# Optimization experiments

Measured on AMD Instinct MI355X. Metric: run time of the kernel, lower is better.

The kernel has to match this reference:

```python
import jax, jax.numpy as jnp
import numpy as np

N = 100000   # nodes
E = 3200000  # edges
G = 256      # graphs in batch
C_IN, H, OUT = 5, 64, 2
EPS = 1e-5


def setup_inputs() -> dict:
    key = jax.random.key(0)
    ks = jax.random.split(key, 16)
    d = {
        "x": jax.random.normal(ks[0], (N, C_IN), jnp.float32),
        "edge_index": jax.random.randint(ks[1], (2, E), 0, N, jnp.int64),
        "batch": jnp.sort(jax.random.randint(ks[2], (N,), 0, G, jnp.int64)),
        "W1": jax.random.normal(ks[3], (C_IN, H), jnp.float32),
        "b1": jax.random.normal(ks[4], (H,), jnp.float32),
        "g1": jax.random.uniform(ks[5], (H,), jnp.float32),
        "be1": jax.random.normal(ks[6], (H,), jnp.float32),
        "rm1": jnp.zeros((H,), jnp.float32),
        "rv1": jnp.ones((H,), jnp.float32),
        "W2": jax.random.normal(ks[7], (H, H), jnp.float32),
        "b2": jax.random.normal(ks[8], (H,), jnp.float32),
        "g2": jax.random.uniform(ks[9], (H,), jnp.float32),
        "be2": jax.random.normal(ks[10], (H,), jnp.float32),
        "rm2": jnp.zeros((H,), jnp.float32),
        "rv2": jnp.ones((H,), jnp.float32),
        "W3": jax.random.normal(ks[11], (H, H), jnp.float32),
        "b3": jax.random.normal(ks[12], (H,), jnp.float32),
        "g3": jax.random.uniform(ks[13], (H,), jnp.float32),
        "be3": jax.random.normal(ks[14], (H,), jnp.float32),
        "rm3": jnp.zeros((H,), jnp.float32),
        "rv3": jnp.ones((H,), jnp.float32),
        "Wf1": jax.random.normal(ks[15], (H, 32), jnp.float32),
        "bf1": jax.random.normal(jax.random.fold_in(key, 1), (32,), jnp.float32),
        "Wf2": jax.random.normal(jax.random.fold_in(key, 2), (32, OUT), jnp.float32),
        "bf2": jax.random.normal(jax.random.fold_in(key, 3), (OUT,), jnp.float32),
    }
    return d


def reference(x, edge_index, batch, W1, b1, g1, be1, rm1, rv1,
              W2, b2, g2, be2, rm2, rv2, W3, b3, g3, be3, rm3, rv3,
              Wf1, bf1, Wf2, bf2):
    src, dst = edge_index[0], edge_index[1]
    # GCN symmetric normalization with self-loops: deg includes the self edge
    deg = jax.ops.segment_sum(jnp.ones((E,), x.dtype), dst, num_segments=N) + 1.0
    dinv = jax.lax.rsqrt(deg)            # [N]
    enorm = dinv[src] * dinv[dst]        # per-edge norm  [E]
    snorm = dinv * dinv                  # self-loop norm [N]

    def gcn(h, W, b):
        h = h @ W                                                  # [N,H]
        agg = jax.ops.segment_sum(h[src] * enorm[:, None], dst, num_segments=N)
        return agg + h * snorm[:, None] + b

    def bn(h, g, be, rm, rv):  # eval-mode BatchNorm1d
        return (h - rm) * jax.lax.rsqrt(rv + EPS) * g + be

    h = jax.nn.relu(bn(gcn(x, W1, b1), g1, be1, rm1, rv1))
    h = jax.nn.relu(bn(gcn(h, W2, b2), g2, be2, rm2, rv2))
    h = jax.nn.relu(bn(gcn(h, W3, b3), g3, be3, rm3, rv3))

    counts = jax.ops.segment_sum(jnp.ones((N,), h.dtype), batch, num_segments=G)
    pooled = jax.ops.segment_sum(h, batch, num_segments=G) / jnp.maximum(counts, 1.0)[:, None]

    h = jax.nn.relu(pooled @ Wf1 + bf1)  # dropout is identity in eval
    return jax.nn.sigmoid(h @ Wf2 + bf2)
```

## Files before the change

### kernel.cpp

```cpp
#include <hip/hip_runtime.h>
#include <hip/hip_bf16.h>

#define HF 64
#define EPS 1e-5f

#define BSH 9
#define BKN (1 << BSH)
#define NBUCK_MAX 256
#define PB_T 256
#define PB_EPT 32
#define PB_TILE (PB_T * PB_EPT)

#define LGRID 2048

typedef __hip_bfloat16 bf16;

__device__ __forceinline__ unsigned char f32_to_fp8(float v) {
    int p = __builtin_amdgcn_cvt_pk_fp8_f32(v, v, 0, false);
    return (unsigned char)(p & 0xff);
}

__device__ __forceinline__ float rdlane(float v, int k) {
    return __int_as_float(__builtin_amdgcn_readlane(__float_as_int(v), k));
}

__device__ __forceinline__ unsigned bf16_rne_hi(float x) {
    unsigned u = __float_as_uint(x);
    return (u + 0x7fffu + ((u >> 16) & 1u)) & 0xffff0000u;
}

__global__ __launch_bounds__(PB_T) void k_bhist(const int* __restrict__ dst,
                                                int* __restrict__ bcnt, int E, int B) {
    __shared__ int bh[NBUCK_MAX];
    int t = threadIdx.x;
    for (int b = t; b < B; b += PB_T) bh[b] = 0;
    __syncthreads();
    int tile0 = blockIdx.x * PB_TILE;
#pragma unroll
    for (int k = 0; k < PB_EPT; ++k) {
        int e = tile0 + k * PB_T + t;
        if (e < E) atomicAdd(&bh[dst[e] >> BSH], 1);
    }
    __syncthreads();
    for (int b = t; b < B; b += PB_T) {
        int c = bh[b];
        if (c) atomicAdd(&bcnt[b], c);
    }
}

__global__ void k_bscan(const int* __restrict__ bcnt, int* __restrict__ bbase2,
                        int* __restrict__ bcur, int* __restrict__ base, int B, int N, int E) {
    if (threadIdx.x == 0 && blockIdx.x == 0) {
        int acc = 0;
        for (int i = 0; i < B; ++i) { bbase2[i] = acc; bcur[i] = acc; acc += bcnt[i]; }
        bbase2[B] = acc;
        base[N] = E;
    }
}

__global__ __launch_bounds__(PB_T) void k_passB(
    const int* __restrict__ src, const int* __restrict__ dst,
    int* __restrict__ bcur, int* __restrict__ stage, int E, int B) {
    __shared__ int scnt[NBUCK_MAX];
    __shared__ int sgoff[NBUCK_MAX];
    int t = threadIdx.x;
    int tile0 = blockIdx.x * PB_TILE;

    for (int b = t; b < B; b += PB_T) scnt[b] = 0;
    __syncthreads();

    int rec[PB_EPT];
    int bkt[PB_EPT];
#pragma unroll
    for (int k = 0; k < PB_EPT; ++k) {
        int e = tile0 + k * PB_T + t;
        bkt[k] = -1;
        if (e < E) {
            int d = dst[e];
            int s = src[e];
            int b = d >> BSH;
            bkt[k] = b;
            rec[k] = s | ((d & (BKN - 1)) << 17);
            atomicAdd(&scnt[b], 1);
        }
    }
    __syncthreads();

    for (int b = t; b < B; b += PB_T) {
        int c = scnt[b];
        sgoff[b] = c ? atomicAdd(&bcur[b], c) : 0;
        scnt[b] = 0;
    }
    __syncthreads();

#pragma unroll
    for (int k = 0; k < PB_EPT; ++k) {
        if (bkt[k] >= 0) {
            int loc = atomicAdd(&scnt[bkt[k]], 1);
            stage[sgoff[bkt[k]] + loc] = rec[k];
        }
    }
}

__global__ __launch_bounds__(512) void k_passC(const int* __restrict__ stage,
                                               const int* __restrict__ bb2,
                                               int* __restrict__ base,
                                               float* __restrict__ dinv,
                                               int* __restrict__ csr, int N) {
    __shared__ int lcnt[BKN];
    __shared__ int lscan[BKN];
    __shared__ int lcur[BKN];
    int beta = blockIdx.x;
    int n0 = beta * BKN;
    int n1 = n0 + BKN; if (n1 > N) n1 = N;
    int nn = n1 - n0;
    int t = threadIdx.x;
    lcnt[t] = 0;
    __syncthreads();
    int rbeg = bb2[beta], rend = bb2[beta + 1];
    for (int i = rbeg + t; i < rend; i += 512)
        atomicAdd(&lcnt[stage[i] >> 17], 1);
    __syncthreads();
    int v = lcnt[t];
    lscan[t] = v;
    __syncthreads();
    for (int off = 1; off < 512; off <<= 1) {
        int val = lscan[t];
        int add = (t >= off) ? lscan[t - off] : 0;
        __syncthreads();
        lscan[t] = val + add;
        __syncthreads();
    }
    int b = rbeg + lscan[t] - v;
    if (t < nn) {
        base[n0 + t] = b;
        dinv[n0 + t] = rsqrtf((float)v + 1.0f);
    }
    lcur[t] = b;
    __syncthreads();
    for (int i = rbeg + t; i < rend; i += 512) {
        int r = stage[i];
        int pos = atomicAdd(&lcur[r >> 17], 1);
        csr[pos] = r & 0x1ffff;
    }
}

__global__ void k_prescale(const float* __restrict__ x, const float* __restrict__ dinv,
                           float* __restrict__ xs, int N5) {
    int i = blockIdx.x * blockDim.x + threadIdx.x;
    if (i < N5) xs[i] = x[i] * dinv[i / 5];
}

__global__ __launch_bounds__(256) void k_layer1(
    const float* __restrict__ xs, unsigned char* __restrict__ hout,
    const int* __restrict__ csr, const int* __restrict__ basep,
    const float* __restrict__ dinv,
    const float* __restrict__ W1, const float* __restrict__ b,
    const float* __restrict__ g, const float* __restrict__ be,
    const float* __restrict__ rm, const float* __restrict__ rv, int N) {
    __shared__ float sW[5 * HF];
    __shared__ float sB[HF];
    __shared__ float sScale[HF];
    if (threadIdx.x < HF) {
        int f = threadIdx.x;
        float scale = g[f] * rsqrtf(rv[f] + EPS);
        sScale[f] = scale;
        sB[f] = (b[f] - rm[f]) * scale + be[f];
    }
    __syncthreads();
    for (int i = threadIdx.x; i < 5 * HF; i += blockDim.x)
        sW[i] = W1[i] * sScale[i & (HF - 1)];
    __syncthreads();

    int lane = threadIdx.x & 63;
    int wave = threadIdx.x >> 6;
    int c  = lane & 7;
    int g8 = lane >> 3;
    int stride = gridDim.x * 4;

    for (int node = blockIdx.x * 4 + wave; node < N; node += stride) {
        int j   = __builtin_amdgcn_readfirstlane(basep[node]);
        int end = __builtin_amdgcn_readfirstlane(basep[node + 1]);

        float a0 = 0.f, a1 = 0.f, a2 = 0.f, a3 = 0.f;
        if (g8 == 0 && c < 5) a0 = xs[node * 5 + c];

        for (; j + 32 <= end; j += 32) {
            int s0 = csr[j + g8];
            int s1 = csr[j + 8 + g8];
            int s2 = csr[j + 16 + g8];
            int s3 = csr[j + 24 + g8];
            float v0 = xs[s0 * 5 + c];
            float v1 = xs[s1 * 5 + c];
            float v2 = xs[s2 * 5 + c];
            float v3 = xs[s3 * 5 + c];
            a0 += v0; a1 += v1; a2 += v2; a3 += v3;
        }
        for (; j + 8 <= end; j += 8) {
            int s = csr[j + g8];
            a0 += xs[s * 5 + c];
        }
        if (j < end) {
            if (j + g8 < end) {
                int s = csr[j + g8];
                a0 += xs[s * 5 + c];
            }
        }

        float acc = (a0 + a1) + (a2 + a3);
        acc += __shfl_xor(acc, 8, 64);
        acc += __shfl_xor(acc, 16, 64);
        acc += __shfl_xor(acc, 32, 64);

        float di = dinv[node];
        acc *= di;

        float out = sB[lane];
#pragma unroll
        for (int k = 0; k < 5; ++k) out += __shfl(acc, k, 64) * sW[k * HF + lane];
        out = fmaxf(out, 0.f);
        hout[(size_t)node * HF + lane] = f32_to_fp8(out * di);
    }
}

template <int SCALE_OUT>
__global__ __launch_bounds__(256, 4) void k_layer(
    const unsigned char* __restrict__ hs8, void* __restrict__ hout_v,
    const int* __restrict__ csr, const int* __restrict__ basep,
    const float* __restrict__ dinv,
    const float* __restrict__ W, const float* __restrict__ b,
    const float* __restrict__ g, const float* __restrict__ be,
    const float* __restrict__ rm, const float* __restrict__ rv, int N) {
    int lane = threadIdx.x & 63;
    int wave = threadIdx.x >> 6;
    int stride = gridDim.x * 4;
    const unsigned char* col = hs8 + lane;

    float scale = g[lane] * rsqrtf(rv[lane] + EPS);
    float bias  = (b[lane] - rm[lane]) * scale + be[lane];
    unsigned wp[HF / 2];
#pragma unroll
    for (int k2 = 0; k2 < HF / 2; ++k2) {
        unsigned lo = bf16_rne_hi(W[(2 * k2 + 0) * HF + lane] * scale);
        unsigned hi = bf16_rne_hi(W[(2 * k2 + 1) * HF + lane] * scale);
        wp[k2] = (lo >> 16) | hi;
    }

    for (int node = blockIdx.x * 4 + wave; node < N; node += stride) {
        int j   = __builtin_amdgcn_readfirstlane(basep[node]);
        int end = __builtin_amdgcn_readfirstlane(basep[node + 1]);

        float a0 = __builtin_amdgcn_cvt_f32_fp8((unsigned)col[(size_t)node * HF], 0);
        float a1 = 0.f, a2 = 0.f, a3 = 0.f;

        for (; j + 16 <= end; j += 16) {
            int s0 = csr[j+0],  s1 = csr[j+1],  s2 = csr[j+2],  s3 = csr[j+3];
            int s4 = csr[j+4],  s5 = csr[j+5],  s6 = csr[j+6],  s7 = csr[j+7];
            int s8 = csr[j+8],  s9 = csr[j+9],  sA = csr[j+10], sB_ = csr[j+11];
            int sC = csr[j+12], sD = csr[j+13], sE = csr[j+14], sF = csr[j+15];
            unsigned u0 = col[(size_t)s0 * HF];
            unsigned u1 = col[(size_t)s1 * HF];
            unsigned u2 = col[(size_t)s2 * HF];
            unsigned u3 = col[(size_t)s3 * HF];
            unsigned u4 = col[(size_t)s4 * HF];
            unsigned u5 = col[(size_t)s5 * HF];
            unsigned u6 = col[(size_t)s6 * HF];
            unsigned u7 = col[(size_t)s7 * HF];
            unsigned u8 = col[(size_t)s8 * HF];
            unsigned u9 = col[(size_t)s9 * HF];
            unsigned uA = col[(size_t)sA * HF];
            unsigned uB = col[(size_t)sB_ * HF];
            unsigned uC = col[(size_t)sC * HF];
            unsigned uD = col[(size_t)sD * HF];
            unsigned uE = col[(size_t)sE * HF];
            unsigned uF = col[(size_t)sF * HF];
            a0 += __builtin_amdgcn_cvt_f32_fp8(u0, 0);
            a1 += __builtin_amdgcn_cvt_f32_fp8(u1, 0);
            a2 += __builtin_amdgcn_cvt_f32_fp8(u2, 0);
            a3 += __builtin_amdgcn_cvt_f32_fp8(u3, 0);
            a0 += __builtin_amdgcn_cvt_f32_fp8(u4, 0);
            a1 += __builtin_amdgcn_cvt_f32_fp8(u5, 0);
            a2 += __builtin_amdgcn_cvt_f32_fp8(u6, 0);
            a3 += __builtin_amdgcn_cvt_f32_fp8(u7, 0);
            a0 += __builtin_amdgcn_cvt_f32_fp8(u8, 0);
            a1 += __builtin_amdgcn_cvt_f32_fp8(u9, 0);
            a2 += __builtin_amdgcn_cvt_f32_fp8(uA, 0);
            a3 += __builtin_amdgcn_cvt_f32_fp8(uB, 0);
            a0 += __builtin_amdgcn_cvt_f32_fp8(uC, 0);
            a1 += __builtin_amdgcn_cvt_f32_fp8(uD, 0);
            a2 += __builtin_amdgcn_cvt_f32_fp8(uE, 0);
            a3 += __builtin_amdgcn_cvt_f32_fp8(uF, 0);
        }
        for (; j + 4 <= end; j += 4) {
            int s0 = csr[j+0], s1 = csr[j+1], s2 = csr[j+2], s3 = csr[j+3];
            unsigned u0 = col[(size_t)s0 * HF];
            unsigned u1 = col[(size_t)s1 * HF];
            unsigned u2 = col[(size_t)s2 * HF];
            unsigned u3 = col[(size_t)s3 * HF];
            a0 += __builtin_amdgcn_cvt_f32_fp8(u0, 0);
            a1 += __builtin_amdgcn_cvt_f32_fp8(u1, 0);
            a2 += __builtin_amdgcn_cvt_f32_fp8(u2, 0);
            a3 += __builtin_amdgcn_cvt_f32_fp8(u3, 0);
        }
        for (; j < end; ++j) {
            int s = csr[j];
            a0 += __builtin_amdgcn_cvt_f32_fp8((unsigned)col[(size_t)s * HF], 0);
        }
        float di = dinv[node];
        float acc = ((a0 + a1) + (a2 + a3)) * di;

        float o0 = bias, o1 = 0.f, o2 = 0.f, o3 = 0.f;
#pragma unroll
        for (int k = 0; k < HF; k += 4) {
            unsigned pA = wp[k / 2 + 0];
            unsigned pB = wp[k / 2 + 1];
            o0 += rdlane(acc, k + 0) * __uint_as_float(pA << 16);
            o1 += rdlane(acc, k + 1) * __uint_as_float(pA & 0xffff0000u);
            o2 += rdlane(acc, k + 2) * __uint_as_float(pB << 16);
            o3 += rdlane(acc, k + 3) * __uint_as_float(pB & 0xffff0000u);
        }
        float out = fmaxf((o0 + o1) + (o2 + o3), 0.f);
        if (SCALE_OUT) {
            ((unsigned char*)hout_v)[(size_t)node * HF + lane] = f32_to_fp8(out * di);
        } else {
            ((float*)hout_v)[(size_t)node * HF + lane] = out;
        }
    }
}

__global__ void k_pool_fc(const float* __restrict__ h, const int* __restrict__ batch,
                          const float* __restrict__ Wf1, const float* __restrict__ bf1,
                          const float* __restrict__ Wf2, const float* __restrict__ bf2,
                          float* __restrict__ out, int N) {
    int g = blockIdx.x;
    int t = threadIdx.x;
    int f = t & 63, q = t >> 6;

    int lo = 0, hi = N;
    while (lo < hi) { int mid = (lo + hi) >> 1; if (batch[mid] < g) lo = mid + 1; else hi = mid; }
    int start = lo;
    hi = N;
    while (lo < hi) { int mid = (lo + hi) >> 1; if (batch[mid] < g + 1) lo = mid + 1; else hi = mid; }
    int end = lo;

    float sum = 0.f;
    for (int n = start + q; n < end; n += 4) sum += h[n * HF + f];

    __shared__ float red[4][HF];
    __shared__ float sp[HF];
    __shared__ float sh[32];
    red[q][f] = sum;
    __syncthreads();
    if (q == 0) {
        float s = red[0][f] + red[1][f] + red[2][f] + red[3][f];
        float cntf = (float)(end - start);
        sp[f] = s / fmaxf(cntf, 1.0f);
    }
    __syncthreads();
    if (t < 32) {
        float a = bf1[t];
#pragma unroll
        for (int k = 0; k < HF; ++k) a += sp[k] * Wf1[k * 32 + t];
        sh[t] = fmaxf(a, 0.f);
    }
    __syncthreads();
    if (t < 2) {
        float a = bf2[t];
#pragma unroll
        for (int k = 0; k < 32; ++k) a += sh[k] * Wf2[k * 2 + t];
        out[g * 2 + t] = 1.f / (1.f + expf(-a));
    }
}

extern "C" void kernel_launch(void* const* d_in, const int* in_sizes, int n_in,
                              void* d_out, int out_size, void* d_ws, size_t ws_size,
                              hipStream_t stream) {
    const float* x     = (const float*)d_in[0];
    const int*   ei    = (const int*)d_in[1];
    const int*   batch = (const int*)d_in[2];
    const float* W1 = (const float*)d_in[3];
    const float* b1 = (const float*)d_in[4];
    const float* g1 = (const float*)d_in[5];
    const float* be1 = (const float*)d_in[6];
    const float* rm1 = (const float*)d_in[7];
    const float* rv1 = (const float*)d_in[8];
    const float* W2 = (const float*)d_in[9];
    const float* b2 = (const float*)d_in[10];
    const float* g2 = (const float*)d_in[11];
    const float* be2 = (const float*)d_in[12];
    const float* rm2 = (const float*)d_in[13];
    const float* rv2 = (const float*)d_in[14];
    const float* W3 = (const float*)d_in[15];
    const float* b3 = (const float*)d_in[16];
    const float* g3 = (const float*)d_in[17];
    const float* be3 = (const float*)d_in[18];
    const float* rm3 = (const float*)d_in[19];
    const float* rv3 = (const float*)d_in[20];
    const float* Wf1 = (const float*)d_in[21];
    const float* bf1 = (const float*)d_in[22];
    const float* Wf2 = (const float*)d_in[23];
    const float* bf2 = (const float*)d_in[24];
    float* out = (float*)d_out;

    const int N = in_sizes[2];
    const int E = in_sizes[1] / 2;
    const int G = out_size / 2;
    const int B = (N + BKN - 1) / BKN;

    char* ws = (char*)d_ws;
    size_t off = 0;
    auto alloc = [&](size_t bytes) {
        char* p = ws + off;
        off += (bytes + 255) & ~(size_t)255;
        return p;
    };
    float*         H3       = (float*)alloc((size_t)N * HF * sizeof(float));
    unsigned char* HS1      = (unsigned char*)alloc((size_t)N * HF);
    unsigned char* HS2      = (unsigned char*)alloc((size_t)N * HF);
    float*         xs       = (float*)alloc((size_t)N * 5 * sizeof(float) + 64);
    float*         dinv     = (float*)alloc((size_t)N * sizeof(float));
    int*           base     = (int*)  alloc(((size_t)N + 1) * sizeof(int));
    int*           bcnt     = (int*)  alloc((size_t)NBUCK_MAX * sizeof(int));
    int*           bbase2   = (int*)  alloc(((size_t)NBUCK_MAX + 1) * sizeof(int));
    int*           bcur     = (int*)  alloc((size_t)NBUCK_MAX * sizeof(int));
    int*           csr      = (int*)  alloc((size_t)E * sizeof(int));
    int*           stage    = (int*)H3;

    const int* src = ei;
    const int* dst = ei + E;

    const int BT = 256;
    int gP  = (N * 5 + BT - 1) / BT;
    int gPB = (E + PB_TILE - 1) / PB_TILE;

    hipMemsetAsync(bcnt, 0, (size_t)B * sizeof(int), stream);
    k_bhist<<<gPB, PB_T, 0, stream>>>(dst, bcnt, E, B);
    k_bscan<<<1, 64, 0, stream>>>(bcnt, bbase2, bcur, base, B, N, E);
    k_passB<<<gPB, PB_T, 0, stream>>>(src, dst, bcur, stage, E, B);
    k_passC<<<B, 512, 0, stream>>>(stage, bbase2, base, dinv, csr, N);
    k_prescale<<<gP, BT, 0, stream>>>(x, dinv, xs, N * 5);

    k_layer1<<<LGRID, BT, 0, stream>>>(xs, HS1, csr, base, dinv,
                                       W1, b1, g1, be1, rm1, rv1, N);
    k_layer<1><<<LGRID, BT, 0, stream>>>(HS1, HS2, csr, base, dinv,
                                         W2, b2, g2, be2, rm2, rv2, N);
    k_layer<0><<<LGRID, BT, 0, stream>>>(HS2, H3, csr, base, dinv,
                                         W3, b3, g3, be3, rm3, rv3, N);

    k_pool_fc<<<G, BT, 0, stream>>>(H3, batch, Wf1, bf1, Wf2, bf2, out, N);
}
```

Measured before the change: 459.6 us.

## Software-pipeline GCN layer gather with deferred MLP and LDS-resident weights

Packed bf16 weights move from 32 per-lane registers into a swizzled shared-memory table, freeing registers. The gather loop changes to 8-wide with register double-buffering, so the next batch's loads are issued before the previous batch is accumulated. Each node's 64x64 transform and store are deferred until after the next node's first gather batch has been issued, overlapping MLP math with memory latency. The cost is LDS reads inside the MLP, extra live state carried across iterations, and a shorter unroll than the previous 16-wide loop.

```diff
diff --git a/kernel.cpp b/kernel.cpp
--- a/kernel.cpp
+++ b/kernel.cpp
@@ -231,20 +231,59 @@
     const float* __restrict__ W, const float* __restrict__ b,
     const float* __restrict__ g, const float* __restrict__ be,
     const float* __restrict__ rm, const float* __restrict__ rv, int N) {
+    __shared__ uint4 swp4[64][8];
+
     int lane = threadIdx.x & 63;
     int wave = threadIdx.x >> 6;
     int stride = gridDim.x * 4;
     const unsigned char* col = hs8 + lane;
 
+    if (threadIdx.x < 64) {
+        int l = threadIdx.x;
+        float sc = g[l] * rsqrtf(rv[l] + EPS);
+#pragma unroll
+        for (int c = 0; c < 8; ++c) {
+            unsigned p[4];
+#pragma unroll
+            for (int q = 0; q < 4; ++q) {
+                int k2 = c * 4 + q;
+                unsigned lo = bf16_rne_hi(W[(2 * k2 + 0) * HF + l] * sc);
+                unsigned hi = bf16_rne_hi(W[(2 * k2 + 1) * HF + l] * sc);
+                p[q] = (lo >> 16) | hi;
+            }
+            swp4[l][c ^ (l & 7)] = make_uint4(p[0], p[1], p[2], p[3]);
+        }
+    }
+    __syncthreads();
+
     float scale = g[lane] * rsqrtf(rv[lane] + EPS);
     float bias  = (b[lane] - rm[lane]) * scale + be[lane];
-    unsigned wp[HF / 2];
-#pragma unroll
-    for (int k2 = 0; k2 < HF / 2; ++k2) {
-        unsigned lo = bf16_rne_hi(W[(2 * k2 + 0) * HF + lane] * scale);
-        unsigned hi = bf16_rne_hi(W[(2 * k2 + 1) * HF + lane] * scale);
-        wp[k2] = (lo >> 16) | hi;
-    }
+
+    auto mlp_store = [&](float acc, int nodeS, float diS) {
+        float o0 = bias, o1 = 0.f, o2 = 0.f, o3 = 0.f;
+#pragma unroll
+        for (int c = 0; c < 8; ++c) {
+            uint4 pv = swp4[lane][c ^ (lane & 7)];
+            int k0 = c * 8;
+            o0 += rdlane(acc, k0 + 0) * __uint_as_float(pv.x << 16);
+            o1 += rdlane(acc, k0 + 1) * __uint_as_float(pv.x & 0xffff0000u);
+            o2 += rdlane(acc, k0 + 2) * __uint_as_float(pv.y << 16);
+            o3 += rdlane(acc, k0 + 3) * __uint_as_float(pv.y & 0xffff0000u);
+            o0 += rdlane(acc, k0 + 4) * __uint_as_float(pv.z << 16);
+            o1 += rdlane(acc, k0 + 5) * __uint_as_float(pv.z & 0xffff0000u);
+            o2 += rdlane(acc, k0 + 6) * __uint_as_float(pv.w << 16);
+            o3 += rdlane(acc, k0 + 7) * __uint_as_float(pv.w & 0xffff0000u);
+        }
+        float out = fmaxf((o0 + o1) + (o2 + o3), 0.f);
+        if (SCALE_OUT) {
+            ((unsigned char*)hout_v)[(size_t)nodeS * HF + lane] = f32_to_fp8(out * diS);
+        } else {
+            ((float*)hout_v)[(size_t)nodeS * HF + lane] = out;
+        }
+    };
+
+    float accP = 0.f, diP = 0.f;
+    int nodeP = -1;
 
     for (int node = blockIdx.x * 4 + wave; node < N; node += stride) {
         int j   = __builtin_amdgcn_readfirstlane(basep[node]);
@@ -253,27 +292,44 @@
         float a0 = __builtin_amdgcn_cvt_f32_fp8((unsigned)col[(size_t)node * HF], 0);
         float a1 = 0.f, a2 = 0.f, a3 = 0.f;
 
-        for (; j + 16 <= end; j += 16) {
-            int s0 = csr[j+0],  s1 = csr[j+1],  s2 = csr[j+2],  s3 = csr[j+3];
-            int s4 = csr[j+4],  s5 = csr[j+5],  s6 = csr[j+6],  s7 = csr[j+7];
-            int s8 = csr[j+8],  s9 = csr[j+9],  sA = csr[j+10], sB_ = csr[j+11];
-            int sC = csr[j+12], sD = csr[j+13], sE = csr[j+14], sF = csr[j+15];
-            unsigned u0 = col[(size_t)s0 * HF];
-            unsigned u1 = col[(size_t)s1 * HF];
-            unsigned u2 = col[(size_t)s2 * HF];
-            unsigned u3 = col[(size_t)s3 * HF];
-            unsigned u4 = col[(size_t)s4 * HF];
-            unsigned u5 = col[(size_t)s5 * HF];
-            unsigned u6 = col[(size_t)s6 * HF];
-            unsigned u7 = col[(size_t)s7 * HF];
-            unsigned u8 = col[(size_t)s8 * HF];
-            unsigned u9 = col[(size_t)s9 * HF];
-            unsigned uA = col[(size_t)sA * HF];
-            unsigned uB = col[(size_t)sB_ * HF];
-            unsigned uC = col[(size_t)sC * HF];
-            unsigned uD = col[(size_t)sD * HF];
-            unsigned uE = col[(size_t)sE * HF];
-            unsigned uF = col[(size_t)sF * HF];
+        unsigned u0 = 0, u1 = 0, u2 = 0, u3 = 0, u4 = 0, u5 = 0, u6 = 0, u7 = 0;
+        bool w0 = (j + 8 <= end);
+        if (w0) {
+            int s0 = csr[j+0], s1 = csr[j+1], s2 = csr[j+2], s3 = csr[j+3];
+            int s4 = csr[j+4], s5 = csr[j+5], s6 = csr[j+6], s7 = csr[j+7];
+            u0 = col[(size_t)s0 * HF]; u1 = col[(size_t)s1 * HF];
+            u2 = col[(size_t)s2 * HF]; u3 = col[(size_t)s3 * HF];
+            u4 = col[(size_t)s4 * HF]; u5 = col[(size_t)s5 * HF];
+            u6 = col[(size_t)s6 * HF]; u7 = col[(size_t)s7 * HF];
+        }
+
+        if (nodeP >= 0) mlp_store(accP, nodeP, diP);
+
+        if (w0) {
+            j += 8;
+            while (j + 8 <= end) {
+                int t0 = csr[j+0], t1 = csr[j+1], t2 = csr[j+2], t3 = csr[j+3];
+                int t4 = csr[j+4], t5 = csr[j+5], t6 = csr[j+6], t7 = csr[j+7];
+                unsigned v0 = col[(size_t)t0 * HF];
+                unsigned v1 = col[(size_t)t1 * HF];
+                unsigned v2 = col[(size_t)t2 * HF];
+                unsigned v3 = col[(size_t)t3 * HF];
+                unsigned v4 = col[(size_t)t4 * HF];
+                unsigned v5 = col[(size_t)t5 * HF];
+                unsigned v6 = col[(size_t)t6 * HF];
+                unsigned v7 = col[(size_t)t7 * HF];
+                a0 += __builtin_amdgcn_cvt_f32_fp8(u0, 0);
+                a1 += __builtin_amdgcn_cvt_f32_fp8(u1, 0);
+                a2 += __builtin_amdgcn_cvt_f32_fp8(u2, 0);
+                a3 += __builtin_amdgcn_cvt_f32_fp8(u3, 0);
+                a0 += __builtin_amdgcn_cvt_f32_fp8(u4, 0);
+                a1 += __builtin_amdgcn_cvt_f32_fp8(u5, 0);
+                a2 += __builtin_amdgcn_cvt_f32_fp8(u6, 0);
+                a3 += __builtin_amdgcn_cvt_f32_fp8(u7, 0);
+                u0 = v0; u1 = v1; u2 = v2; u3 = v3;
+                u4 = v4; u5 = v5; u6 = v6; u7 = v7;
+                j += 8;
+            }
             a0 += __builtin_amdgcn_cvt_f32_fp8(u0, 0);
             a1 += __builtin_amdgcn_cvt_f32_fp8(u1, 0);
             a2 += __builtin_amdgcn_cvt_f32_fp8(u2, 0);
@@ -282,50 +338,18 @@
             a1 += __builtin_amdgcn_cvt_f32_fp8(u5, 0);
             a2 += __builtin_amdgcn_cvt_f32_fp8(u6, 0);
             a3 += __builtin_amdgcn_cvt_f32_fp8(u7, 0);
-            a0 += __builtin_amdgcn_cvt_f32_fp8(u8, 0);
-            a1 += __builtin_amdgcn_cvt_f32_fp8(u9, 0);
-            a2 += __builtin_amdgcn_cvt_f32_fp8(uA, 0);
-            a3 += __builtin_amdgcn_cvt_f32_fp8(uB, 0);
-            a0 += __builtin_amdgcn_cvt_f32_fp8(uC, 0);
-            a1 += __builtin_amdgcn_cvt_f32_fp8(uD, 0);
-            a2 += __builtin_amdgcn_cvt_f32_fp8(uE, 0);
-            a3 += __builtin_amdgcn_cvt_f32_fp8(uF, 0);
-        }
-        for (; j + 4 <= end; j += 4) {
-            int s0 = csr[j+0], s1 = csr[j+1], s2 = csr[j+2], s3 = csr[j+3];
-            unsigned u0 = col[(size_t)s0 * HF];
-            unsigned u1 = col[(size_t)s1 * HF];
-            unsigned u2 = col[(size_t)s2 * HF];
-            unsigned u3 = col[(size_t)s3 * HF];
-            a0 += __builtin_amdgcn_cvt_f32_fp8(u0, 0);
-            a1 += __builtin_amdgcn_cvt_f32_fp8(u1, 0);
-            a2 += __builtin_amdgcn_cvt_f32_fp8(u2, 0);
-            a3 += __builtin_amdgcn_cvt_f32_fp8(u3, 0);
         }
         for (; j < end; ++j) {
             int s = csr[j];
             a0 += __builtin_amdgcn_cvt_f32_fp8((unsigned)col[(size_t)s * HF], 0);
         }
+
         float di = dinv[node];
-        float acc = ((a0 + a1) + (a2 + a3)) * di;
-
-        float o0 = bias, o1 = 0.f, o2 = 0.f, o3 = 0.f;
-#pragma unroll
-        for (int k = 0; k < HF; k += 4) {
-            unsigned pA = wp[k / 2 + 0];
-            unsigned pB = wp[k / 2 + 1];
-            o0 += rdlane(acc, k + 0) * __uint_as_float(pA << 16);
-            o1 += rdlane(acc, k + 1) * __uint_as_float(pA & 0xffff0000u);
-            o2 += rdlane(acc, k + 2) * __uint_as_float(pB << 16);
-            o3 += rdlane(acc, k + 3) * __uint_as_float(pB & 0xffff0000u);
-        }
-        float out = fmaxf((o0 + o1) + (o2 + o3), 0.f);
-        if (SCALE_OUT) {
-            ((unsigned char*)hout_v)[(size_t)node * HF + lane] = f32_to_fp8(out * di);
-        } else {
-            ((float*)hout_v)[(size_t)node * HF + lane] = out;
-        }
-    }
+        accP = ((a0 + a1) + (a2 + a3)) * di;
+        diP = di;
+        nodeP = node;
+    }
+    if (nodeP >= 0) mlp_store(accP, nodeP, diP);
 }
 
 __global__ void k_pool_fc(const float* __restrict__ h, const int* __restrict__ batch,
```

New measurement: 427.5 us. -7.0%, faster.
